# Optimization experiments

Measured on AMD Instinct MI355X. Metric: run time of the kernel, lower is better.

The kernel has to match this reference:

```python
import jax, jax.numpy as jnp
import numpy as np

SCALING = 32.0 / 16  # alpha / rank


def setup_inputs() -> dict:
    key = jax.random.key(0)
    k1, k2, k3, k4, k5 = jax.random.split(key, 5)
    B, S, IN, OUT, R = 4, 2048, 4096, 4096, 16
    x = jax.random.normal(k1, (B, S, IN), dtype=jnp.float32)
    weight = jax.random.normal(k2, (OUT, IN), dtype=jnp.float32) * 0.02
    lora_a_w = jax.random.normal(k3, (R, IN), dtype=jnp.float32) * 0.02
    lora_b_w = jax.random.normal(k4, (OUT, R), dtype=jnp.float32) * 0.02
    magnitude = jax.random.uniform(k5, (OUT,), dtype=jnp.float32) + 0.5
    return {"x": x, "weight": weight, "lora_a_w": lora_a_w,
            "lora_b_w": lora_b_w, "magnitude": magnitude}


def reference(x, weight, lora_a_w, lora_b_w, magnitude):
    # base linear: x @ W^T  -> [..., out_dim]
    base_out = jnp.einsum('bsi,oi->bso', x, weight)
    # low-rank path (dropout is identity at p=0.0)
    lora_out = jnp.einsum('bsr,or->bso', jnp.einsum('bsi,ri->bsr', x, lora_a_w), lora_b_w)
    # merged low-rank weight B @ A (torch uses an eye-matrix trick; direct matmul is equivalent)
    lora_weight = lora_b_w @ lora_a_w  # [out, in]
    # row-wise norm of adapted weight; detached in the original
    weight_norm = jax.lax.stop_gradient(
        jnp.linalg.norm(weight + SCALING * lora_weight, axis=1))  # [out]
    mag_norm_scale = (magnitude / weight_norm)[None, None, :]  # [1,1,out]
    dora_out = (mag_norm_scale - 1.0) * base_out + mag_norm_scale * lora_out * SCALING
    return dora_out + base_out
```

## Files before the change

### kernel.cpp

```cpp
#include <hip/hip_runtime.h>
#include <hip/hip_bf16.h>
#include <stdint.h>

#define M_DIM 8192
#define N_DIM 4096
#define K_DIM 4096
#define R_DIM 16
#define NT    64

#define WROWS    32
#define WBLOCKS  (N_DIM / WROWS)
#define CAST_BLOCKS 4096

typedef __attribute__((ext_vector_type(8))) short bf16x8;
typedef __attribute__((ext_vector_type(4))) float f32x4;

__device__ __forceinline__ unsigned short f2bf(float f) {
  union { float f; unsigned int u; } v; v.f = f;
  unsigned int r = 0x7FFFu + ((v.u >> 16) & 1u);
  return (unsigned short)((v.u + r) >> 16);
}

__device__ __forceinline__ void gload16(const unsigned short* g, unsigned short* l) {
  __builtin_amdgcn_global_load_lds(
      (const __attribute__((address_space(1))) void*)g,
      (__attribute__((address_space(3))) void*)l,
      16, 0, 0);
}

__global__ void __launch_bounds__(256) prep_kernel(
    const float4* __restrict__ x4, ushort4* __restrict__ xbf4,
    const float4* __restrict__ W4, const float4* __restrict__ Aw4,
    const float* __restrict__ Bw, const float* __restrict__ mag,
    ushort4* __restrict__ wbf4, float* __restrict__ scale) {
  const int tid = threadIdx.x;
  __shared__ float BoL[WROWS * R_DIM];
  __shared__ float red[4][WROWS];

  if (blockIdx.x >= WBLOCKS) {
    const int base = (blockIdx.x - WBLOCKS) * 2048 + tid;
    #pragma unroll
    for (int u = 0; u < 8; ++u) {
      const int i = base + u * 256;
      float4 f = x4[i];
      ushort4 o;
      o.x = f2bf(f.x); o.y = f2bf(f.y); o.z = f2bf(f.z); o.w = f2bf(f.w);
      xbf4[i] = o;
    }
    return;
  }

  const int o0 = blockIdx.x * WROWS;
  for (int i = tid; i < WROWS * R_DIM; i += 256)
    BoL[i] = Bw[o0 * R_DIM + i] * 2.0f;
  __syncthreads();

  float ssa[WROWS];
  #pragma unroll
  for (int r = 0; r < WROWS; ++r) ssa[r] = 0.f;

  for (int ch = 0; ch < 4; ++ch) {
    const int c = ch * 256 + tid;
    float4 a[R_DIM];
    #pragma unroll
    for (int r = 0; r < R_DIM; ++r) a[r] = Aw4[(size_t)r * 1024 + c];

    #pragma unroll
    for (int row = 0; row < WROWS; ++row) {
      float4 v = W4[(size_t)(o0 + row) * 1024 + c];
      const float4 b0 = *(const float4*)&BoL[row * R_DIM + 0];
      const float4 b1 = *(const float4*)&BoL[row * R_DIM + 4];
      const float4 b2 = *(const float4*)&BoL[row * R_DIM + 8];
      const float4 b3 = *(const float4*)&BoL[row * R_DIM + 12];
#define FMA4(bb, ar) { v.x += (bb)*(ar).x; v.y += (bb)*(ar).y; v.z += (bb)*(ar).z; v.w += (bb)*(ar).w; }
      FMA4(b0.x, a[0])  FMA4(b0.y, a[1])  FMA4(b0.z, a[2])  FMA4(b0.w, a[3])
      FMA4(b1.x, a[4])  FMA4(b1.y, a[5])  FMA4(b1.z, a[6])  FMA4(b1.w, a[7])
      FMA4(b2.x, a[8])  FMA4(b2.y, a[9])  FMA4(b2.z, a[10]) FMA4(b2.w, a[11])
      FMA4(b3.x, a[12]) FMA4(b3.y, a[13]) FMA4(b3.z, a[14]) FMA4(b3.w, a[15])
#undef FMA4
      ssa[row] += v.x * v.x + v.y * v.y + v.z * v.z + v.w * v.w;
      ushort4 ov;
      ov.x = f2bf(v.x); ov.y = f2bf(v.y); ov.z = f2bf(v.z); ov.w = f2bf(v.w);
      wbf4[(size_t)(o0 + row) * 1024 + c] = ov;
    }
  }

  const int lane = tid & 63;
  const int wave = tid >> 6;
  #pragma unroll
  for (int row = 0; row < WROWS; ++row) {
    float v = ssa[row];
    #pragma unroll
    for (int off = 32; off > 0; off >>= 1) v += __shfl_down(v, off, 64);
    if (lane == 0) red[wave][row] = v;
  }
  __syncthreads();
  if (tid < WROWS) {
    const float s = red[0][tid] + red[1][tid] + red[2][tid] + red[3][tid];
    scale[o0 + tid] = mag[o0 + tid] / sqrtf(s);
  }
}

#define VMCNT_(n) asm volatile("s_waitcnt vmcnt(" #n ")" ::: "memory")
#define VMCNT(n) VMCNT_(n)

__global__ void __launch_bounds__(512, 2)
dora_gemm(const unsigned short* __restrict__ A,
          const unsigned short* __restrict__ Bt,
          const float* __restrict__ scale,
          float* __restrict__ C) {
  __shared__ __align__(16) unsigned short As[2][2][128 * 64];
  __shared__ __align__(16) unsigned short Bs[2][2][128 * 64];

  const int tid  = threadIdx.x;
  const int lane = tid & 63;
  const int wave = tid >> 6;

  const int fid = blockIdx.y * gridDim.x + blockIdx.x;
  const int s   = (fid & 7) * 64 + (fid >> 3);
  const int bM  = (s >> 4) * 256;
  const int bN  = (s & 15) * 256;

  const int l3  = lane >> 3;
  const int l7  = lane & 7;
  const int swz = (l7 ^ l3) * 8;
  const int w8  = wave * 8;

  const unsigned short* srcA = A  + (size_t)(bM + w8 + l3) * K_DIM + swz;
  const unsigned short* srcB = Bt + (size_t)(bN + (wave & 3) * 8 + l3 + 64 * (wave >> 2)) * K_DIM + swz;

  const int fr   = lane & 15;
  const int fq   = lane >> 4;
  const int fr7  = fr & 7;
  const int arow = fr + 64 * (wave >> 2);
  const int brow = fr + 32 * (wave & 3);

  f32x4 acc[8][4];
  #pragma unroll
  for (int i = 0; i < 8; ++i)
    #pragma unroll
    for (int j = 0; j < 4; ++j) acc[i][j] = (f32x4){0.f, 0.f, 0.f, 0.f};

  bf16x8 aF[4][2];
  bf16x8 bF0[2][2];
  bf16x8 bF1[2][2];

#define STAGE_A(cc, hh, k0) do {                                              \
    gload16(srcA + (size_t)((hh) * 64)       * K_DIM + (k0), (unsigned short*)&As[cc][hh][w8 * 64]);        \
    gload16(srcA + (size_t)((hh) * 64 + 128) * K_DIM + (k0), (unsigned short*)&As[cc][hh][(64 + w8) * 64]); \
  } while (0)
#define STAGE_B(cc, hh, k0) do {                                              \
    gload16(srcB + (size_t)((hh) * 32)       * K_DIM + (k0), (unsigned short*)&Bs[cc][hh][w8 * 64]);        \
    gload16(srcB + (size_t)((hh) * 32 + 128) * K_DIM + (k0), (unsigned short*)&Bs[cc][hh][(64 + w8) * 64]); \
  } while (0)
#define LOAD_A(cc, mh) do {                                                   \
    _Pragma("unroll")                                                         \
    for (int mt = 0; mt < 4; ++mt) {                                          \
      _Pragma("unroll")                                                       \
      for (int h = 0; h < 2; ++h)                                             \
        aF[mt][h] = *(const bf16x8*)&As[cc][mh][(arow + mt * 16) * 64 + (((h * 4 + fq) ^ fr7) * 8)]; \
    }                                                                         \
  } while (0)
#define LOAD_B(cc, nh, dst) do {                                              \
    _Pragma("unroll")                                                         \
    for (int nt = 0; nt < 2; ++nt) {                                          \
      _Pragma("unroll")                                                       \
      for (int h = 0; h < 2; ++h)                                             \
        dst[nt][h] = *(const bf16x8*)&Bs[cc][nh][(brow + nt * 16) * 64 + (((h * 4 + fq) ^ fr7) * 8)]; \
    }                                                                         \
  } while (0)
#define MFMA_Q(mh, nh, bfr) do {                                              \
    _Pragma("unroll")                                                         \
    for (int mt = 0; mt < 4; ++mt) {                                          \
      _Pragma("unroll")                                                       \
      for (int nt = 0; nt < 2; ++nt) {                                        \
        _Pragma("unroll")                                                     \
        for (int h = 0; h < 2; ++h)                                           \
          acc[(mh) * 4 + mt][(nh) * 2 + nt] = __builtin_amdgcn_mfma_f32_16x16x32_bf16( \
              aF[mt][h], bfr[nt][h], acc[(mh) * 4 + mt][(nh) * 2 + nt], 0, 0, 0); \
      }                                                                       \
    }                                                                         \
  } while (0)
#define PH_SYNC_IN()  do { __builtin_amdgcn_s_barrier();                      \
    asm volatile("s_waitcnt lgkmcnt(0)" ::: "memory"); } while (0)
#define PRIO1 __builtin_amdgcn_s_setprio(1)
#define PRIO0 __builtin_amdgcn_s_setprio(0)

#define GROUP(cc, tt, STG, W1N, W4N) do {                                     \
                                                                      \
    LOAD_A(cc, 0); LOAD_B(cc, 0, bF0);                                        \
    PH_SYNC_IN();                                                             \
    PRIO1; MFMA_Q(0, 0, bF0); PRIO0;                                          \
    VMCNT(W1N);                                                               \
    __builtin_amdgcn_s_barrier();                                             \
                                                                      \
    LOAD_B(cc, 1, bF1);                                                       \
    if (STG) STAGE_A(cc, 0, ((tt) + 2) * 64);                                 \
    PH_SYNC_IN();                                                             \
    PRIO1; MFMA_Q(0, 1, bF1); PRIO0;                                          \
    __builtin_amdgcn_s_barrier();                                             \
                                                                      \
    LOAD_A(cc, 1);                                                            \
    if (STG) STAGE_B(cc, 0, ((tt) + 2) * 64);                                 \
    PH_SYNC_IN();                                                             \
    PRIO1; MFMA_Q(1, 0, bF0); PRIO0;                                          \
    __builtin_amdgcn_s_barrier();                                             \
                                                                      \
    if (STG) { STAGE_A(cc, 1, ((tt) + 2) * 64); STAGE_B(cc, 1, ((tt) + 2) * 64); } \
    PH_SYNC_IN();                                                             \
    PRIO1; MFMA_Q(1, 1, bF1); PRIO0;                                          \
    VMCNT(W4N);                                                               \
    __builtin_amdgcn_s_barrier();                                             \
  } while (0)

  STAGE_A(0, 0, 0);  STAGE_B(0, 0, 0);
  STAGE_A(0, 1, 0);  STAGE_B(0, 1, 0);
  STAGE_A(1, 0, 64); STAGE_B(1, 0, 64);
  STAGE_A(1, 1, 64); STAGE_B(1, 1, 64);
  VMCNT(12);
  __builtin_amdgcn_s_barrier();

  for (int t = 0; t < NT - 2; t += 2) {
    GROUP(0, t, 1, 8, 12);
    GROUP(1, t + 1, 1, 8, 12);
  }
  GROUP(0, NT - 2, 0, 8, 4);
  GROUP(1, NT - 1, 0, 0, 0);

#undef GROUP
#undef PRIO0
#undef PRIO1
#undef PH_SYNC_IN
#undef MFMA_Q
#undef LOAD_B
#undef LOAD_A
#undef STAGE_B
#undef STAGE_A

  const int wMo = (wave >> 2) * 128;
  const int wNo = (wave & 3) * 64;
  float scv[4];
  #pragma unroll
  for (int fn = 0; fn < 4; ++fn) scv[fn] = scale[bN + wNo + fn * 16 + fr];
  #pragma unroll
  for (int fm = 0; fm < 8; ++fm) {
    const int m0 = bM + wMo + fm * 16 + fq * 4;
    #pragma unroll
    for (int fn = 0; fn < 4; ++fn) {
      const int n = bN + wNo + fn * 16 + fr;
      #pragma unroll
      for (int r = 0; r < 4; ++r)
        C[(size_t)(m0 + r) * N_DIM + n] = acc[fm][fn][r] * scv[fn];
    }
  }
}

extern "C" void kernel_launch(void* const* d_in, const int* in_sizes, int n_in,
                              void* d_out, int out_size, void* d_ws, size_t ws_size,
                              hipStream_t stream) {
  const float* x   = (const float*)d_in[0];
  const float* W   = (const float*)d_in[1];
  const float* la  = (const float*)d_in[2];
  const float* lb  = (const float*)d_in[3];
  const float* mag = (const float*)d_in[4];
  float* out = (float*)d_out;

  unsigned short* xbf = (unsigned short*)d_ws;
  unsigned short* wbf = (unsigned short*)((char*)d_ws + (size_t)M_DIM * K_DIM * 2);
  float* scale = (float*)((char*)d_ws + (size_t)M_DIM * K_DIM * 2 + (size_t)N_DIM * K_DIM * 2);

  prep_kernel<<<WBLOCKS + CAST_BLOCKS, 256, 0, stream>>>(
      (const float4*)x, (ushort4*)xbf, (const float4*)W, (const float4*)la,
      lb, mag, (ushort4*)wbf, scale);
  dim3 grid(N_DIM / 256, M_DIM / 256);
  dora_gemm<<<grid, 512, 0, stream>>>(xbf, wbf, scale, out);
}
```

Before: 661.3 us.

## Software-pipeline LDS fragment loads behind MFMAs and shrink weight-norm block rows

Restructures the GEMM main loop so LDS fragment reads for the next quadrant (and the next K-tile's first A/B fragments) are issued between MFMA halves instead of before an explicit lgkmcnt(0) wait. The A fragments are split into low/high halves so loads can interleave with compute, and the per-phase order is changed so bF1 is reused across two quadrants. The explicit LDS waits are dropped and the vmcnt thresholds are retuned. Separately, the weight-norm kernel now uses 8 rows per block instead of 32 for more blocks and fewer registers, and its chunk loop is no longer unrolled. Relying on compiler-inserted waits risks ordering hazards or extra stalls.

After: 557.0 us. -15.8%, faster.

```diff
diff --git a/kernel.cpp b/kernel.cpp
--- a/kernel.cpp
+++ b/kernel.cpp
@@ -8,7 +8,7 @@
 #define R_DIM 16
 #define NT    64
 
-#define WROWS    32
+#define WROWS    8
 #define WBLOCKS  (N_DIM / WROWS)
 #define CAST_BLOCKS 4096
 
@@ -51,14 +51,14 @@
   }
 
   const int o0 = blockIdx.x * WROWS;
-  for (int i = tid; i < WROWS * R_DIM; i += 256)
-    BoL[i] = Bw[o0 * R_DIM + i] * 2.0f;
+  if (tid < WROWS * R_DIM) BoL[tid] = Bw[o0 * R_DIM + tid] * 2.0f;
   __syncthreads();
 
   float ssa[WROWS];
   #pragma unroll
   for (int r = 0; r < WROWS; ++r) ssa[r] = 0.f;
 
+  #pragma unroll 1
   for (int ch = 0; ch < 4; ++ch) {
     const int c = ch * 256 + tid;
     float4 a[R_DIM];
@@ -141,7 +141,7 @@
     #pragma unroll
     for (int j = 0; j < 4; ++j) acc[i][j] = (f32x4){0.f, 0.f, 0.f, 0.f};
 
-  bf16x8 aF[4][2];
+  bf16x8 aLo[2][2], aHi[2][2];
   bf16x8 bF0[2][2];
   bf16x8 bF1[2][2];
 
@@ -153,13 +153,19 @@
     gload16(srcB + (size_t)((hh) * 32)       * K_DIM + (k0), (unsigned short*)&Bs[cc][hh][w8 * 64]);        \
     gload16(srcB + (size_t)((hh) * 32 + 128) * K_DIM + (k0), (unsigned short*)&Bs[cc][hh][(64 + w8) * 64]); \
   } while (0)
-#define LOAD_A(cc, mh) do {                                                   \
-    _Pragma("unroll")                                                         \
-    for (int mt = 0; mt < 4; ++mt) {                                          \
+#define LOAD_A_LO(cc, mh) do {                                                \
+    _Pragma("unroll")                                                         \
+    for (int mi = 0; mi < 2; ++mi)                                            \
       _Pragma("unroll")                                                       \
       for (int h = 0; h < 2; ++h)                                             \
-        aF[mt][h] = *(const bf16x8*)&As[cc][mh][(arow + mt * 16) * 64 + (((h * 4 + fq) ^ fr7) * 8)]; \
-    }                                                                         \
+        aLo[mi][h] = *(const bf16x8*)&As[cc][mh][(arow + mi * 16) * 64 + (((h * 4 + fq) ^ fr7) * 8)]; \
+  } while (0)
+#define LOAD_A_HI(cc, mh) do {                                                \
+    _Pragma("unroll")                                                         \
+    for (int mi = 0; mi < 2; ++mi)                                            \
+      _Pragma("unroll")                                                       \
+      for (int h = 0; h < 2; ++h)                                             \
+        aHi[mi][h] = *(const bf16x8*)&As[cc][mh][(arow + (mi + 2) * 16) * 64 + (((h * 4 + fq) ^ fr7) * 8)]; \
   } while (0)
 #define LOAD_B(cc, nh, dst) do {                                              \
     _Pragma("unroll")                                                         \
@@ -169,71 +175,71 @@
         dst[nt][h] = *(const bf16x8*)&Bs[cc][nh][(brow + nt * 16) * 64 + (((h * 4 + fq) ^ fr7) * 8)]; \
     }                                                                         \
   } while (0)
-#define MFMA_Q(mh, nh, bfr) do {                                              \
-    _Pragma("unroll")                                                         \
-    for (int mt = 0; mt < 4; ++mt) {                                          \
+#define MFMA_PAIR(mh, nh, bfr, aARR, mtb) do {                                \
+    _Pragma("unroll")                                                         \
+    for (int mi = 0; mi < 2; ++mi) {                                          \
       _Pragma("unroll")                                                       \
       for (int nt = 0; nt < 2; ++nt) {                                        \
         _Pragma("unroll")                                                     \
         for (int h = 0; h < 2; ++h)                                           \
-          acc[(mh) * 4 + mt][(nh) * 2 + nt] = __builtin_amdgcn_mfma_f32_16x16x32_bf16( \
-              aF[mt][h], bfr[nt][h], acc[(mh) * 4 + mt][(nh) * 2 + nt], 0, 0, 0); \
+          acc[(mh) * 4 + (mtb) + mi][(nh) * 2 + nt] = __builtin_amdgcn_mfma_f32_16x16x32_bf16( \
+              aARR[mi][h], bfr[nt][h], acc[(mh) * 4 + (mtb) + mi][(nh) * 2 + nt], 0, 0, 0); \
       }                                                                       \
     }                                                                         \
   } while (0)
-#define PH_SYNC_IN()  do { __builtin_amdgcn_s_barrier();                      \
-    asm volatile("s_waitcnt lgkmcnt(0)" ::: "memory"); } while (0)
+#define BAR   __builtin_amdgcn_s_barrier()
 #define PRIO1 __builtin_amdgcn_s_setprio(1)
 #define PRIO0 __builtin_amdgcn_s_setprio(0)
 
-#define GROUP(cc, tt, STG, W1N, W4N) do {                                     \
-                                                                      \
-    LOAD_A(cc, 0); LOAD_B(cc, 0, bF0);                                        \
-    PH_SYNC_IN();                                                             \
-    PRIO1; MFMA_Q(0, 0, bF0); PRIO0;                                          \
-    VMCNT(W1N);                                                               \
-    __builtin_amdgcn_s_barrier();                                             \
-                                                                      \
+#define GROUP(cc, tt, STG, W3, NX) do {                                       \
+                                       \
     LOAD_B(cc, 1, bF1);                                                       \
+    PRIO1; MFMA_PAIR(0, 0, bF0, aLo, 0); MFMA_PAIR(0, 0, bF0, aHi, 2); PRIO0; \
+    BAR;                                                                      \
+                  \
     if (STG) STAGE_A(cc, 0, ((tt) + 2) * 64);                                 \
-    PH_SYNC_IN();                                                             \
-    PRIO1; MFMA_Q(0, 1, bF1); PRIO0;                                          \
-    __builtin_amdgcn_s_barrier();                                             \
-                                                                      \
-    LOAD_A(cc, 1);                                                            \
+    PRIO1; MFMA_PAIR(0, 1, bF1, aLo, 0); PRIO0;                               \
+    LOAD_A_LO(cc, 1);                                                         \
+    PRIO1; MFMA_PAIR(0, 1, bF1, aHi, 2); PRIO0;                               \
+    LOAD_A_HI(cc, 1);                                                         \
+    BAR;                                                                      \
+                          \
     if (STG) STAGE_B(cc, 0, ((tt) + 2) * 64);                                 \
-    PH_SYNC_IN();                                                             \
-    PRIO1; MFMA_Q(1, 0, bF0); PRIO0;                                          \
-    __builtin_amdgcn_s_barrier();                                             \
-                                                                      \
+    PRIO1; MFMA_PAIR(1, 1, bF1, aLo, 0); MFMA_PAIR(1, 1, bF1, aHi, 2); PRIO0; \
+    VMCNT(W3);                                                                \
+    BAR;                                                                      \
+             \
     if (STG) { STAGE_A(cc, 1, ((tt) + 2) * 64); STAGE_B(cc, 1, ((tt) + 2) * 64); } \
-    PH_SYNC_IN();                                                             \
-    PRIO1; MFMA_Q(1, 1, bF1); PRIO0;                                          \
-    VMCNT(W4N);                                                               \
-    __builtin_amdgcn_s_barrier();                                             \
+    PRIO1; MFMA_PAIR(1, 0, bF0, aLo, 0); PRIO0;                               \
+    if (NX) LOAD_A_LO((cc) ^ 1, 0);                                           \
+    PRIO1; MFMA_PAIR(1, 0, bF0, aHi, 2); PRIO0;                               \
+    if (NX) { LOAD_A_HI((cc) ^ 1, 0); LOAD_B((cc) ^ 1, 0, bF0); }             \
+    BAR;                                                                      \
   } while (0)
 
   STAGE_A(0, 0, 0);  STAGE_B(0, 0, 0);
   STAGE_A(0, 1, 0);  STAGE_B(0, 1, 0);
   STAGE_A(1, 0, 64); STAGE_B(1, 0, 64);
   STAGE_A(1, 1, 64); STAGE_B(1, 1, 64);
-  VMCNT(12);
-  __builtin_amdgcn_s_barrier();
+  VMCNT(8);
+  BAR;
+  LOAD_A_LO(0, 0); LOAD_A_HI(0, 0); LOAD_B(0, 0, bF0);
 
   for (int t = 0; t < NT - 2; t += 2) {
-    GROUP(0, t, 1, 8, 12);
-    GROUP(1, t + 1, 1, 8, 12);
-  }
-  GROUP(0, NT - 2, 0, 8, 4);
+    GROUP(0, t,     1, 4, 1);
+    GROUP(1, t + 1, 1, 4, 1);
+  }
+  GROUP(0, NT - 2, 0, 0, 1);
   GROUP(1, NT - 1, 0, 0, 0);
 
 #undef GROUP
 #undef PRIO0
 #undef PRIO1
-#undef PH_SYNC_IN
-#undef MFMA_Q
+#undef BAR
+#undef MFMA_PAIR
 #undef LOAD_B
-#undef LOAD_A
+#undef LOAD_A_HI
+#undef LOAD_A_LO
 #undef STAGE_B
 #undef STAGE_A
 
```
